# Optimization experiments

Measured on AMD Instinct MI355X. Metric: run time of the kernel, lower is better.

Reference implementation:

```python
import jax, jax.numpy as jnp
import numpy as np

N_HEADS = 16
HEAD = 64
HID = 1024
WIN = 256
LN_EPS = 1e-5


def _ln(x, g, b):
    m = jnp.mean(x, axis=-1, keepdims=True)
    v = jnp.mean((x - m) ** 2, axis=-1, keepdims=True)
    return (x - m) * jax.lax.rsqrt(v + LN_EPS) * g + b


def _window_shift(x):
    return jnp.concatenate([jnp.zeros_like(x[:, :WIN]), x[:, :-WIN]], axis=1)


def _additive_attn(x, vec, mask_add):
    B, S, _ = x.shape
    # per-head logits: (x * vec) summed within each head, scaled
    attn = (x * vec).reshape(B, S, N_HEADS, HEAD).sum(-1) / (HEAD ** 0.5)
    attn = jnp.exp(attn + mask_add)[..., None]          # [B,S,H,1]
    xh = x.reshape(B, S, N_HEADS, HEAD)
    s = jnp.cumsum(attn * xh, axis=1)
    s = s - _window_shift(s)                             # windowed cumsum of attn*x
    z = jnp.cumsum(attn, axis=1)
    z = z - _window_shift(z)                             # windowed cumsum of attn
    return (s / z).reshape(B, S, HID)


def setup_inputs():
    key = jax.random.key(0)
    ks = jax.random.split(key, 7)
    B, S = 4, 4096
    w = lambda k: (jax.random.normal(k, (HID, HID)) * 0.02).astype(jnp.float32)
    return {
        "hidden_states": jax.random.normal(ks[0], (B, S, HID), dtype=jnp.float32),
        "attention_mask": jnp.ones((B, S), dtype=jnp.float32),
        "Wq": w(ks[1]), "Wk": w(ks[2]), "Wv": w(ks[3]), "Wp": w(ks[4]),
        "query_attn": (jax.random.normal(ks[5], (HID,)) * 0.02).astype(jnp.float32),
        "key_attn": (jax.random.normal(ks[6], (HID,)) * 0.02).astype(jnp.float32),
        "ln1_g": jnp.ones((HID,), jnp.float32), "ln1_b": jnp.zeros((HID,), jnp.float32),
        "ln2_g": jnp.ones((HID,), jnp.float32), "ln2_b": jnp.zeros((HID,), jnp.float32),
    }


def reference(hidden_states, attention_mask, Wq, Wk, Wv, Wp, query_attn, key_attn,
              ln1_g, ln1_b, ln2_g, ln2_b):
    h = _ln(hidden_states, ln1_g, ln1_b)
    query = h @ Wq.T
    keys = h @ Wk.T
    values = h @ Wv.T
    mask_add = ((1.0 - attention_mask) * -10000.0)[:, :, None]  # [B,S,1]
    pooled_q = _additive_attn(query, query_attn, mask_add)
    pooled_q = pooled_q @ Wp.T                                  # (dropout is identity in eval)
    residual = h + pooled_q * keys
    mixed = _ln(residual, ln2_g, ln2_b)
    pooled_k = _additive_attn(mixed, key_attn, mask_add)
    return residual + pooled_k * values
```

## Files before the change

kernel.cpp:

```cpp
#include <hip/hip_runtime.h>
#include <hip/hip_bf16.h>

#define HID 1024
#define NH 16
#define HEAD 64
#define WIN 256
#define SEQ 4096
#define BATCH 4
#define NROWS (BATCH * SEQ)
#define LN_EPS 1e-5f

typedef unsigned short u16;
typedef __bf16 bf16x8 __attribute__((ext_vector_type(8)));
typedef float f32x4 __attribute__((ext_vector_type(4)));

static __device__ inline float bfu(u16 u) {
    union { unsigned int i; float f; } x;
    x.i = ((unsigned int)u) << 16;
    return x.f;
}

static __device__ inline u16 f2bf(float f) {
    union { float f; unsigned int i; } x;
    x.f = f;
    unsigned int lsb = (x.i >> 16) & 1u;
    x.i += 0x7fffu + lsb;
    return (u16)(x.i >> 16);
}

__global__ __launch_bounds__(256) void convert_weights(
    const float* __restrict__ wq, const float* __restrict__ wk,
    const float* __restrict__ wv, const float* __restrict__ wp,
    u16* __restrict__ o)
{
    int i = blockIdx.x * 256 + threadIdx.x;
    const int n = 1024 * 1024;
    if (i < n) {
        o[i]         = f2bf(wq[i]);
        o[n + i]     = f2bf(wk[i]);
        o[2 * n + i] = f2bf(wv[i]);
        o[3 * n + i] = f2bf(wp[i]);
    }
}

__global__ __launch_bounds__(256) void ln1_kernel(
    const float* __restrict__ x, const float* __restrict__ g,
    const float* __restrict__ b, u16* __restrict__ out)
{
    int row = blockIdx.x;
    int t = threadIdx.x;
    float4 v = ((const float4*)(x + (size_t)row * HID))[t];
    float s  = v.x + v.y + v.z + v.w;
    float ss = v.x * v.x + v.y * v.y + v.z * v.z + v.w * v.w;
    __shared__ float red[8];
    #pragma unroll
    for (int off = 32; off; off >>= 1) { s += __shfl_down(s, off); ss += __shfl_down(ss, off); }
    int wave = t >> 6, lane = t & 63;
    if (lane == 0) { red[wave] = s; red[4 + wave] = ss; }
    __syncthreads();
    float S  = red[0] + red[1] + red[2] + red[3];
    float SS = red[4] + red[5] + red[6] + red[7];
    float mean = S * (1.f / HID);
    float var  = SS * (1.f / HID) - mean * mean;
    float inv  = rsqrtf(var + LN_EPS);
    float4 gv = ((const float4*)g)[t];
    float4 bv = ((const float4*)b)[t];
    ushort4 o;
    o.x = f2bf((v.x - mean) * inv * gv.x + bv.x);
    o.y = f2bf((v.y - mean) * inv * gv.y + bv.y);
    o.z = f2bf((v.z - mean) * inv * gv.z + bv.z);
    o.w = f2bf((v.w - mean) * inv * gv.w + bv.w);
    ((ushort4*)(out + (size_t)row * HID))[t] = o;
}

#define GLDS(gp, lp) __builtin_amdgcn_global_load_lds( \
    (const __attribute__((address_space(1))) void*)(gp), \
    (__attribute__((address_space(3))) void*)(lp), 16, 0, 0)

#define PHASE(MH, KH, LOADB, STAGE_CODE, WAIT_CODE)                            \
  {                                                                            \
    if (LOADB) {                                                               \
      _Pragma("unroll") for (int n = 0; n < 4; ++n)                            \
        bF[n] = *(const bf16x8*)&rB[wc * 4096 +                                \
            (n * 16 + (lane & 15)) * 64 + ((c0 ^ ((KH) << 6)) >> 1)];          \
    }                                                                          \
    bf16x8 aF[4];                                                              \
    _Pragma("unroll") for (int i = 0; i < 4; ++i) {                            \
      const int mf = (MH) * 4 + i;                                             \
      aF[i] = *(const bf16x8*)&rA[(mf >> 1) * 4096 +                           \
          (wr * 32 + (mf & 1) * 16 + (lane & 15)) * 64 +                       \
          ((c0 ^ ((KH) << 6)) >> 1)];                                          \
    }                                                                          \
    STAGE_CODE                                                                 \
    WAIT_CODE                                                                  \
    __builtin_amdgcn_s_barrier();                                              \
    __builtin_amdgcn_sched_barrier(0);                                         \
    __builtin_amdgcn_s_setprio(1);                                             \
    _Pragma("unroll") for (int i = 0; i < 4; ++i)                              \
      _Pragma("unroll") for (int n = 0; n < 4; ++n)                            \
        acc[(MH) * 4 + i][n] = __builtin_amdgcn_mfma_f32_16x16x32_bf16(        \
            aF[i], bF[n], acc[(MH) * 4 + i][n], 0, 0, 0);                      \
    __builtin_amdgcn_s_setprio(0);                                             \
    __builtin_amdgcn_s_barrier();                                              \
    __builtin_amdgcn_sched_barrier(0);                                         \
  }

__global__ __launch_bounds__(512, 2) void gemm256(
    const u16* __restrict__ A, const u16* __restrict__ W,
    u16* __restrict__ C, int K, int ldc)
{
    __shared__ __align__(16) u16 sA[2][256 * 64];
    __shared__ __align__(16) u16 sB[2][256 * 64];

    const int tid = threadIdx.x;
    const int wgl = blockIdx.x >> 3;
    const int bm = (blockIdx.x & 7) * 8 + (wgl & 7);
    const int bn = wgl >> 3;

    const int wave = tid >> 6, lane = tid & 63;
    const int wr = wave >> 2, wc = wave & 3;

    const int rp = tid >> 3;
    const int colE = (((tid & 7) * 16) ^ ((rp & 7) << 4)) >> 1;
    const u16* gA = A + (size_t)(bm * 256 + (rp < 32 ? rp : rp + 96)) * K + colE;
    const u16* gB = W + (size_t)(bn * 256 + rp) * K + colE;

    const int c0 = ((lane >> 4) * 16) ^ ((lane & 7) << 4);

    f32x4 acc[8][4];
    #pragma unroll
    for (int m = 0; m < 8; ++m)
        #pragma unroll
        for (int n = 0; n < 4; ++n) {
            f32x4 z = {0.f, 0.f, 0.f, 0.f};
            acc[m][n] = z;
        }

    const int nk = K >> 6;

    #pragma unroll
    for (int w = 0; w < 4; ++w) GLDS(gB + (size_t)w * 64 * K, &sB[0][w * 4096 + tid * 8]);
    #pragma unroll
    for (int p = 0; p < 4; ++p) GLDS(gA + (size_t)p * 32 * K, &sA[0][p * 4096 + tid * 8]);
    asm volatile("s_waitcnt vmcnt(2)" ::: "memory");
    __builtin_amdgcn_s_barrier();
    __builtin_amdgcn_sched_barrier(0);

    for (int kt = 0; kt < nk; ++kt) {
        const int b = kt & 1;
        const u16* rA = sA[b];
        const u16* rB = sB[b];
        u16* dA = sA[b ^ 1];
        u16* dB = sB[b ^ 1];
        const bool pf = (kt + 1 < nk);
        const size_t ko = (size_t)(kt + 1) * 64;
        bf16x8 bF[4];

        PHASE(0, 0, true,
            { if (pf) { GLDS(gB + ko,                      &dB[0 * 4096 + tid * 8]);
                        GLDS(gB + (size_t)1 * 64 * K + ko, &dB[1 * 4096 + tid * 8]); } },
            { if (pf) asm volatile("s_waitcnt vmcnt(2)" ::: "memory");
              else    asm volatile("s_waitcnt vmcnt(0)" ::: "memory"); })
        PHASE(1, 0, false,
            { if (pf) { GLDS(gB + (size_t)2 * 64 * K + ko, &dB[2 * 4096 + tid * 8]);
                        GLDS(gB + (size_t)3 * 64 * K + ko, &dB[3 * 4096 + tid * 8]); } },
            { })
        PHASE(0, 1, true,
            { if (pf) { GLDS(gA + ko,                      &dA[0 * 4096 + tid * 8]);
                        GLDS(gA + (size_t)1 * 32 * K + ko, &dA[1 * 4096 + tid * 8]); } },
            { })
        PHASE(1, 1, false,
            { if (pf) { GLDS(gA + (size_t)2 * 32 * K + ko, &dA[2 * 4096 + tid * 8]);
                        GLDS(gA + (size_t)3 * 32 * K + ko, &dA[3 * 4096 + tid * 8]); } },
            { if (pf) asm volatile("s_waitcnt vmcnt(2)" ::: "memory"); })
    }

    #pragma unroll
    for (int mf = 0; mf < 8; ++mf) {
        int row0 = bm * 256 + wr * 128 + mf * 16 + ((lane >> 4) << 2);
        #pragma unroll
        for (int n = 0; n < 4; ++n) {
            int col = bn * 256 + wc * 64 + n * 16 + (lane & 15);
            #pragma unroll
            for (int r = 0; r < 4; ++r)
                C[(size_t)(row0 + r) * ldc + col] = f2bf(acc[mf][n][r]);
        }
    }
}

__global__ __launch_bounds__(256) void logits_kernel(
    const u16* __restrict__ x, int xstride,
    const float* __restrict__ vec, const float* __restrict__ mask,
    float* __restrict__ aw)
{
    int h = blockIdx.y, b = blockIdx.z;
    int s = blockIdx.x * 256 + threadIdx.x;
    __shared__ float vl[HEAD];
    if (threadIdx.x < HEAD) vl[threadIdx.x] = vec[h * HEAD + threadIdx.x];
    __syncthreads();
    const uint4* xr = (const uint4*)(x + ((size_t)(b * SEQ + s)) * xstride + h * HEAD);
    float dot = 0.f;
    #pragma unroll
    for (int i = 0; i < 8; ++i) {
        uint4 v = xr[i];
        const u16* p = (const u16*)&v;
        #pragma unroll
        for (int j = 0; j < 8; ++j) dot += bfu(p[j]) * vl[i * 8 + j];
    }
    float ma = (1.0f - mask[b * SEQ + s]) * -10000.0f;
    aw[((size_t)b * NH + h) * SEQ + s] = expf(dot * 0.125f + ma);
}

__global__ __launch_bounds__(256) void attn_win(
    const u16* __restrict__ x, int xstride,
    const float* __restrict__ aw_g,
    u16* __restrict__ out_bf,
    const u16* __restrict__ vsrc,
    float* __restrict__ outF,
    int fused)
{
    int c = blockIdx.x, h = blockIdx.y, b = blockIdx.z;
    __shared__ float awl[2][WIN];
    __shared__ float sts[2][4][HEAD];
    __shared__ float stz[2][4];

    int t = threadIdx.x, wave = t >> 6, lane = t & 63;
    bool havePrev = (c > 0);

    const float* awb = aw_g + ((size_t)b * NH + h) * SEQ;
    for (int i = t; i < 2 * WIN; i += 256) {
        int cc = i >> 8, j = i & (WIN - 1);
        float v = 0.f;
        if (cc == 1) v = awb[c * WIN + j];
        else if (havePrev) v = awb[(c - 1) * WIN + j];
        awl[cc][j] = v;
    }
    __syncthreads();

    const u16* xb = x + (size_t)b * SEQ * xstride + h * HEAD + lane;
    int jp0 = (havePrev ? (c - 1) : c) * WIN;
    int jc0 = c * WIN;
    int j0 = wave << 6;

    float s0 = 0.f, s1 = 0.f, z0 = 0.f, z1 = 0.f;
    #pragma unroll 8
    for (int jj = 0; jj < 64; ++jj) {
        int j = j0 + jj;
        float ap = awl[0][j], ac = awl[1][j];
        float xp = bfu(xb[(size_t)(jp0 + j) * xstride]);
        float xc = bfu(xb[(size_t)(jc0 + j) * xstride]);
        s0 += ap * xp; z0 += ap;
        s1 += ac * xc; z1 += ac;
    }
    sts[0][wave][lane] = s0;
    sts[1][wave][lane] = s1;
    if (lane == 0) { stz[0][wave] = z0; stz[1][wave] = z1; }
    __syncthreads();

    float cs0 = 0.f, cs1 = 0.f, cz0 = 0.f, cz1 = 0.f, tots = 0.f, totz = 0.f;
    #pragma unroll
    for (int w2 = 0; w2 < 4; ++w2) {
        float sp = sts[0][w2][lane], zp = stz[0][w2];
        tots += sp; totz += zp;
        if (w2 < wave) {
            cs0 += sp; cz0 += zp;
            cs1 += sts[1][w2][lane]; cz1 += stz[1][w2];
        }
    }

    float rp = cs0, rc = cs1, rzp = cz0, rzc = cz1;
    size_t obase = ((size_t)b * SEQ + c * WIN) * HID + h * HEAD + lane;
    size_t vbase = ((size_t)b * SEQ + c * WIN) * 3072 + 2048 + h * HEAD + lane;
    #pragma unroll 4
    for (int jj = 0; jj < 64; ++jj) {
        int j = j0 + jj;
        float ap = awl[0][j], ac = awl[1][j];
        float xp = bfu(xb[(size_t)(jp0 + j) * xstride]);
        float xc = bfu(xb[(size_t)(jc0 + j) * xstride]);
        rp += ap * xp; rzp += ap;
        rc += ac * xc; rzc += ac;
        float wv = (rc + tots - rp) / (rzc + totz - rzp);
        if (fused) {
            size_t oi = obase + (size_t)j * HID;
            outF[oi] = outF[oi] + wv * bfu(vsrc[vbase + (size_t)j * 3072]);
        } else {
            out_bf[obase + (size_t)j * HID] = f2bf(wv);
        }
    }
}

__global__ __launch_bounds__(256) void resid_ln2(
    const u16* h, const u16* __restrict__ qkv,
    const float* __restrict__ g, const float* __restrict__ b,
    const float* __restrict__ ka, const float* __restrict__ mask,
    float* __restrict__ residual, u16* mixed, float* __restrict__ aw2)
{
    int row = blockIdx.x;
    int t = threadIdx.x;
    ushort4 h4 = ((const ushort4*)(h + (size_t)row * HID))[t];
    ushort4 p4 = ((const ushort4*)(qkv + (size_t)row * 3072))[t];
    ushort4 k4 = ((const ushort4*)(qkv + (size_t)row * 3072 + 1024))[t];
    float r0 = bfu(h4.x) + bfu(p4.x) * bfu(k4.x);
    float r1 = bfu(h4.y) + bfu(p4.y) * bfu(k4.y);
    float r2 = bfu(h4.z) + bfu(p4.z) * bfu(k4.z);
    float r3 = bfu(h4.w) + bfu(p4.w) * bfu(k4.w);
    ((float4*)(residual + (size_t)row * HID))[t] = make_float4(r0, r1, r2, r3);

    float s  = r0 + r1 + r2 + r3;
    float ss = r0 * r0 + r1 * r1 + r2 * r2 + r3 * r3;
    __shared__ float red[8];
    #pragma unroll
    for (int off = 32; off; off >>= 1) { s += __shfl_down(s, off); ss += __shfl_down(ss, off); }
    int wave = t >> 6, lane = t & 63;
    if (lane == 0) { red[wave] = s; red[4 + wave] = ss; }
    __syncthreads();
    float S  = red[0] + red[1] + red[2] + red[3];
    float SS = red[4] + red[5] + red[6] + red[7];
    float mean = S * (1.f / HID);
    float var  = SS * (1.f / HID) - mean * mean;
    float inv  = rsqrtf(var + LN_EPS);
    float4 gv = ((const float4*)g)[t];
    float4 bv = ((const float4*)b)[t];
    float n0 = (r0 - mean) * inv * gv.x + bv.x;
    float n1 = (r1 - mean) * inv * gv.y + bv.y;
    float n2 = (r2 - mean) * inv * gv.z + bv.z;
    float n3 = (r3 - mean) * inv * gv.w + bv.w;
    ushort4 o;
    o.x = f2bf(n0); o.y = f2bf(n1); o.z = f2bf(n2); o.w = f2bf(n3);
    ((ushort4*)(mixed + (size_t)row * HID))[t] = o;

    float4 kv = ((const float4*)ka)[t];
    float partial = n0 * kv.x + n1 * kv.y + n2 * kv.z + n3 * kv.w;
    partial += __shfl_xor(partial, 1);
    partial += __shfl_xor(partial, 2);
    partial += __shfl_xor(partial, 4);
    partial += __shfl_xor(partial, 8);
    if ((t & 15) == 0) {
        int hh = t >> 4;
        int bb = row >> 12, sl = row & (SEQ - 1);
        float ma = (1.0f - mask[row]) * -10000.0f;
        aw2[((size_t)bb * NH + hh) * SEQ + sl] = expf(partial * 0.125f + ma);
    }
}

extern "C" void kernel_launch(void* const* d_in, const int* in_sizes, int n_in,
                              void* d_out, int out_size, void* d_ws, size_t ws_size,
                              hipStream_t stream)
{
    const float* hidden = (const float*)d_in[0];
    const float* mask   = (const float*)d_in[1];
    const float* Wq     = (const float*)d_in[2];
    const float* Wk     = (const float*)d_in[3];
    const float* Wv     = (const float*)d_in[4];
    const float* Wp     = (const float*)d_in[5];
    const float* qa     = (const float*)d_in[6];
    const float* ka     = (const float*)d_in[7];
    const float* g1     = (const float*)d_in[8];
    const float* b1     = (const float*)d_in[9];
    const float* g2     = (const float*)d_in[10];
    const float* b2     = (const float*)d_in[11];
    float* out = (float*)d_out;

    char* ws = (char*)d_ws;
    u16* wbf = (u16*)ws;       ws += (size_t)4 * 1024 * 1024 * 2;
    u16* hbf = (u16*)ws;       ws += (size_t)NROWS * HID * 2;
    u16* qkv = (u16*)ws;       ws += (size_t)NROWS * 3072 * 2;
    u16* pooled = (u16*)ws;    ws += (size_t)NROWS * HID * 2;
    float* aw1 = (float*)ws;   ws += (size_t)BATCH * NH * SEQ * 4;
    float* aw2 = (float*)ws;

    convert_weights<<<4096, 256, 0, stream>>>(Wq, Wk, Wv, Wp, wbf);
    ln1_kernel<<<NROWS, 256, 0, stream>>>(hidden, g1, b1, hbf);
    gemm256<<<768, 512, 0, stream>>>(hbf, wbf, qkv, HID, 3072);
    logits_kernel<<<dim3(SEQ / 256, NH, BATCH), 256, 0, stream>>>(qkv, 3072, qa, mask, aw1);
    attn_win<<<dim3(SEQ / WIN, NH, BATCH), 256, 0, stream>>>(qkv, 3072, aw1, pooled,
                                                             (const u16*)nullptr, (float*)nullptr, 0);
    gemm256<<<256, 512, 0, stream>>>(pooled, wbf + (size_t)3 * 1024 * 1024, qkv, HID, 3072);
    resid_ln2<<<NROWS, 256, 0, stream>>>(hbf, qkv, g2, b2, ka, mask, out, hbf, aw2);
    attn_win<<<dim3(SEQ / WIN, NH, BATCH), 256, 0, stream>>>(hbf, HID, aw2, pooled,
                                                             qkv, out, 1);
}
```

Before: 329.3 us.

## Fuse LN1 with weight conversion, persistent GEMM, two-head attention, bf16 residual

Merges the weight conversion into the LN1 launch. The QKV GEMM becomes persistent: 256 blocks loop over 768 tiles and prefetch the next tile's first K-slice while writing the current tile's output. The windowed attention kernel now handles two heads per 512-thread block with packed 2-element loads and stores. The residual is stored as bf16 into the free Q slot of qkv instead of a float32 write to the output. The final kernel then writes out in a single pass with no float read-modify-write. The goals are fewer launches, less tail imbalance and less memory traffic. The cost is bf16 rounding of the residual, which adds precision loss to the final output.

```diff
diff --git a/kernel.cpp b/kernel.cpp
--- a/kernel.cpp
+++ b/kernel.cpp
@@ -28,31 +28,28 @@
     return (u16)(x.i >> 16);
 }
 
-__global__ __launch_bounds__(256) void convert_weights(
+__global__ __launch_bounds__(256) void ln1_conv(
+    const float* __restrict__ x, const float* __restrict__ g,
+    const float* __restrict__ b, u16* __restrict__ out,
     const float* __restrict__ wq, const float* __restrict__ wk,
     const float* __restrict__ wv, const float* __restrict__ wp,
-    u16* __restrict__ o)
-{
-    int i = blockIdx.x * 256 + threadIdx.x;
-    const int n = 1024 * 1024;
-    if (i < n) {
-        o[i]         = f2bf(wq[i]);
-        o[n + i]     = f2bf(wk[i]);
-        o[2 * n + i] = f2bf(wv[i]);
-        o[3 * n + i] = f2bf(wp[i]);
-    }
-}
-
-__global__ __launch_bounds__(256) void ln1_kernel(
-    const float* __restrict__ x, const float* __restrict__ g,
-    const float* __restrict__ b, u16* __restrict__ out)
-{
+    u16* __restrict__ wo)
+{
+    __shared__ float red[8];
+    int t = threadIdx.x;
+    if (blockIdx.x >= NROWS) {
+        int i = (blockIdx.x - NROWS) * 256 + t;
+        const int n = 1024 * 1024;
+        wo[i]         = f2bf(wq[i]);
+        wo[n + i]     = f2bf(wk[i]);
+        wo[2 * n + i] = f2bf(wv[i]);
+        wo[3 * n + i] = f2bf(wp[i]);
+        return;
+    }
     int row = blockIdx.x;
-    int t = threadIdx.x;
     float4 v = ((const float4*)(x + (size_t)row * HID))[t];
     float s  = v.x + v.y + v.z + v.w;
     float ss = v.x * v.x + v.y * v.y + v.z * v.z + v.w * v.w;
-    __shared__ float red[8];
     #pragma unroll
     for (int off = 32; off; off >>= 1) { s += __shfl_down(s, off); ss += __shfl_down(ss, off); }
     int wave = t >> 6, lane = t & 63;
@@ -107,84 +104,101 @@
 
 __global__ __launch_bounds__(512, 2) void gemm256(
     const u16* __restrict__ A, const u16* __restrict__ W,
-    u16* __restrict__ C, int K, int ldc)
+    u16* __restrict__ C, int K, int ldc, int ntiles)
 {
     __shared__ __align__(16) u16 sA[2][256 * 64];
     __shared__ __align__(16) u16 sB[2][256 * 64];
 
     const int tid = threadIdx.x;
-    const int wgl = blockIdx.x >> 3;
-    const int bm = (blockIdx.x & 7) * 8 + (wgl & 7);
-    const int bn = wgl >> 3;
-
     const int wave = tid >> 6, lane = tid & 63;
     const int wr = wave >> 2, wc = wave & 3;
 
     const int rp = tid >> 3;
+    const int rowA = (rp < 32 ? rp : rp + 96);
     const int colE = (((tid & 7) * 16) ^ ((rp & 7) << 4)) >> 1;
-    const u16* gA = A + (size_t)(bm * 256 + (rp < 32 ? rp : rp + 96)) * K + colE;
+    const int c0 = ((lane >> 4) * 16) ^ ((lane & 7) << 4);
+
+    const int nk = K >> 6;
+
+    int a = blockIdx.x;
+    int wgl = a >> 3;
+    int bm = (a & 7) * 8 + (wgl & 7);
+    int bn = wgl >> 3;
+    const u16* gA = A + (size_t)(bm * 256 + rowA) * K + colE;
     const u16* gB = W + (size_t)(bn * 256 + rp) * K + colE;
-
-    const int c0 = ((lane >> 4) * 16) ^ ((lane & 7) << 4);
-
-    f32x4 acc[8][4];
-    #pragma unroll
-    for (int m = 0; m < 8; ++m)
+    #pragma unroll
+    for (int w = 0; w < 4; ++w) GLDS(gB + (size_t)w * 64 * K, &sB[0][w * 4096 + tid * 8]);
+    #pragma unroll
+    for (int p = 0; p < 4; ++p) GLDS(gA + (size_t)p * 32 * K, &sA[0][p * 4096 + tid * 8]);
+
+    while (true) {
+        asm volatile("s_waitcnt vmcnt(2)" ::: "memory");
+        __builtin_amdgcn_s_barrier();
+        __builtin_amdgcn_sched_barrier(0);
+
+        f32x4 acc[8][4];
         #pragma unroll
-        for (int n = 0; n < 4; ++n) {
-            f32x4 z = {0.f, 0.f, 0.f, 0.f};
-            acc[m][n] = z;
+        for (int m = 0; m < 8; ++m)
+            #pragma unroll
+            for (int n = 0; n < 4; ++n) {
+                f32x4 z = {0.f, 0.f, 0.f, 0.f};
+                acc[m][n] = z;
+            }
+
+        for (int kt = 0; kt < nk; ++kt) {
+            const int b = kt & 1;
+            const u16* rA = sA[b];
+            const u16* rB = sB[b];
+            u16* dA = sA[b ^ 1];
+            u16* dB = sB[b ^ 1];
+            const bool pf = (kt + 1 < nk);
+            const size_t ko = (size_t)(kt + 1) * 64;
+            bf16x8 bF[4];
+
+            PHASE(0, 0, true,
+                { if (pf) { GLDS(gB + ko,                      &dB[0 * 4096 + tid * 8]);
+                            GLDS(gB + (size_t)1 * 64 * K + ko, &dB[1 * 4096 + tid * 8]); } },
+                { if (pf) asm volatile("s_waitcnt vmcnt(2)" ::: "memory");
+                  else    asm volatile("s_waitcnt vmcnt(0)" ::: "memory"); })
+            PHASE(1, 0, false,
+                { if (pf) { GLDS(gB + (size_t)2 * 64 * K + ko, &dB[2 * 4096 + tid * 8]);
+                            GLDS(gB + (size_t)3 * 64 * K + ko, &dB[3 * 4096 + tid * 8]); } },
+                { })
+            PHASE(0, 1, true,
+                { if (pf) { GLDS(gA + ko,                      &dA[0 * 4096 + tid * 8]);
+                            GLDS(gA + (size_t)1 * 32 * K + ko, &dA[1 * 4096 + tid * 8]); } },
+                { })
+            PHASE(1, 1, false,
+                { if (pf) { GLDS(gA + (size_t)2 * 32 * K + ko, &dA[2 * 4096 + tid * 8]);
+                            GLDS(gA + (size_t)3 * 32 * K + ko, &dA[3 * 4096 + tid * 8]); } },
+                { if (pf) asm volatile("s_waitcnt vmcnt(2)" ::: "memory"); })
         }
 
-    const int nk = K >> 6;
-
-    #pragma unroll
-    for (int w = 0; w < 4; ++w) GLDS(gB + (size_t)w * 64 * K, &sB[0][w * 4096 + tid * 8]);
-    #pragma unroll
-    for (int p = 0; p < 4; ++p) GLDS(gA + (size_t)p * 32 * K, &sA[0][p * 4096 + tid * 8]);
-    asm volatile("s_waitcnt vmcnt(2)" ::: "memory");
-    __builtin_amdgcn_s_barrier();
-    __builtin_amdgcn_sched_barrier(0);
-
-    for (int kt = 0; kt < nk; ++kt) {
-        const int b = kt & 1;
-        const u16* rA = sA[b];
-        const u16* rB = sB[b];
-        u16* dA = sA[b ^ 1];
-        u16* dB = sB[b ^ 1];
-        const bool pf = (kt + 1 < nk);
-        const size_t ko = (size_t)(kt + 1) * 64;
-        bf16x8 bF[4];
-
-        PHASE(0, 0, true,
-            { if (pf) { GLDS(gB + ko,                      &dB[0 * 4096 + tid * 8]);
-                        GLDS(gB + (size_t)1 * 64 * K + ko, &dB[1 * 4096 + tid * 8]); } },
-            { if (pf) asm volatile("s_waitcnt vmcnt(2)" ::: "memory");
-              else    asm volatile("s_waitcnt vmcnt(0)" ::: "memory"); })
-        PHASE(1, 0, false,
-            { if (pf) { GLDS(gB + (size_t)2 * 64 * K + ko, &dB[2 * 4096 + tid * 8]);
-                        GLDS(gB + (size_t)3 * 64 * K + ko, &dB[3 * 4096 + tid * 8]); } },
-            { })
-        PHASE(0, 1, true,
-            { if (pf) { GLDS(gA + ko,                      &dA[0 * 4096 + tid * 8]);
-                        GLDS(gA + (size_t)1 * 32 * K + ko, &dA[1 * 4096 + tid * 8]); } },
-            { })
-        PHASE(1, 1, false,
-            { if (pf) { GLDS(gA + (size_t)2 * 32 * K + ko, &dA[2 * 4096 + tid * 8]);
-                        GLDS(gA + (size_t)3 * 32 * K + ko, &dA[3 * 4096 + tid * 8]); } },
-            { if (pf) asm volatile("s_waitcnt vmcnt(2)" ::: "memory"); })
-    }
-
-    #pragma unroll
-    for (int mf = 0; mf < 8; ++mf) {
-        int row0 = bm * 256 + wr * 128 + mf * 16 + ((lane >> 4) << 2);
+        const int bmC = bm, bnC = bn;
+        a += gridDim.x;
+        const bool more = (a < ntiles);
+        if (more) {
+            wgl = a >> 3; bm = (a & 7) * 8 + (wgl & 7); bn = wgl >> 3;
+            gA = A + (size_t)(bm * 256 + rowA) * K + colE;
+            gB = W + (size_t)(bn * 256 + rp) * K + colE;
+            #pragma unroll
+            for (int w = 0; w < 4; ++w) GLDS(gB + (size_t)w * 64 * K, &sB[0][w * 4096 + tid * 8]);
+            #pragma unroll
+            for (int p = 0; p < 4; ++p) GLDS(gA + (size_t)p * 32 * K, &sA[0][p * 4096 + tid * 8]);
+        }
+
         #pragma unroll
-        for (int n = 0; n < 4; ++n) {
-            int col = bn * 256 + wc * 64 + n * 16 + (lane & 15);
+        for (int mf = 0; mf < 8; ++mf) {
+            int row0 = bmC * 256 + wr * 128 + mf * 16 + ((lane >> 4) << 2);
             #pragma unroll
-            for (int r = 0; r < 4; ++r)
-                C[(size_t)(row0 + r) * ldc + col] = f2bf(acc[mf][n][r]);
+            for (int n = 0; n < 4; ++n) {
+                int col = bnC * 256 + wc * 64 + n * 16 + (lane & 15);
+                #pragma unroll
+                for (int r = 0; r < 4; ++r)
+                    C[(size_t)(row0 + r) * ldc + col] = f2bf(acc[mf][n][r]);
+            }
         }
+        if (!more) break;
     }
 }
 
@@ -211,89 +225,101 @@
     aw[((size_t)b * NH + h) * SEQ + s] = expf(dot * 0.125f + ma);
 }
 
-__global__ __launch_bounds__(256) void attn_win(
+__global__ __launch_bounds__(512) void attn_win2(
     const u16* __restrict__ x, int xstride,
     const float* __restrict__ aw_g,
     u16* __restrict__ out_bf,
-    const u16* __restrict__ vsrc,
+    const u16* __restrict__ resv,
     float* __restrict__ outF,
     int fused)
 {
-    int c = blockIdx.x, h = blockIdx.y, b = blockIdx.z;
-    __shared__ float awl[2][WIN];
-    __shared__ float sts[2][4][HEAD];
-    __shared__ float stz[2][4];
+    int c = blockIdx.x, h2 = blockIdx.y, b = blockIdx.z;
+    __shared__ float awl[2][2][WIN];
+    __shared__ float2 sts[2][8][64];
+    __shared__ float stz[2][8][2];
 
     int t = threadIdx.x, wave = t >> 6, lane = t & 63;
+    int hh = lane >> 5;
+    int coff = hh * 64 + (lane & 31) * 2;
     bool havePrev = (c > 0);
 
-    const float* awb = aw_g + ((size_t)b * NH + h) * SEQ;
-    for (int i = t; i < 2 * WIN; i += 256) {
-        int cc = i >> 8, j = i & (WIN - 1);
+    const float* aw0 = aw_g + ((size_t)b * NH + h2 * 2) * SEQ;
+    for (int i = t; i < 1024; i += 512) {
+        int hd = i >> 9, cc = (i >> 8) & 1, j = i & 255;
         float v = 0.f;
-        if (cc == 1) v = awb[c * WIN + j];
-        else if (havePrev) v = awb[(c - 1) * WIN + j];
-        awl[cc][j] = v;
+        if (cc == 1) v = aw0[hd * SEQ + c * WIN + j];
+        else if (havePrev) v = aw0[hd * SEQ + (c - 1) * WIN + j];
+        awl[hd][cc][j] = v;
     }
     __syncthreads();
 
-    const u16* xb = x + (size_t)b * SEQ * xstride + h * HEAD + lane;
-    int jp0 = (havePrev ? (c - 1) : c) * WIN;
+    const u16* xb = x + (size_t)b * SEQ * xstride + h2 * 128 + coff;
+    int jp0 = (havePrev ? c - 1 : c) * WIN;
     int jc0 = c * WIN;
-    int j0 = wave << 6;
-
-    float s0 = 0.f, s1 = 0.f, z0 = 0.f, z1 = 0.f;
+    int j0 = wave * 32;
+
+    float s0a = 0, s0b = 0, s1a = 0, s1b = 0, z0 = 0, z1 = 0;
     #pragma unroll 8
-    for (int jj = 0; jj < 64; ++jj) {
+    for (int jj = 0; jj < 32; ++jj) {
         int j = j0 + jj;
-        float ap = awl[0][j], ac = awl[1][j];
-        float xp = bfu(xb[(size_t)(jp0 + j) * xstride]);
-        float xc = bfu(xb[(size_t)(jc0 + j) * xstride]);
-        s0 += ap * xp; z0 += ap;
-        s1 += ac * xc; z1 += ac;
-    }
-    sts[0][wave][lane] = s0;
-    sts[1][wave][lane] = s1;
-    if (lane == 0) { stz[0][wave] = z0; stz[1][wave] = z1; }
+        float ap = awl[hh][0][j], ac = awl[hh][1][j];
+        unsigned up = *(const unsigned*)(xb + (size_t)(jp0 + j) * xstride);
+        unsigned uc = *(const unsigned*)(xb + (size_t)(jc0 + j) * xstride);
+        s0a += ap * bfu(up & 0xffff); s0b += ap * bfu(up >> 16); z0 += ap;
+        s1a += ac * bfu(uc & 0xffff); s1b += ac * bfu(uc >> 16); z1 += ac;
+    }
+    sts[0][wave][lane] = make_float2(s0a, s0b);
+    sts[1][wave][lane] = make_float2(s1a, s1b);
+    if ((lane & 31) == 0) { stz[0][wave][hh] = z0; stz[1][wave][hh] = z1; }
     __syncthreads();
 
-    float cs0 = 0.f, cs1 = 0.f, cz0 = 0.f, cz1 = 0.f, tots = 0.f, totz = 0.f;
-    #pragma unroll
-    for (int w2 = 0; w2 < 4; ++w2) {
-        float sp = sts[0][w2][lane], zp = stz[0][w2];
-        tots += sp; totz += zp;
+    float cs0a = 0, cs0b = 0, cs1a = 0, cs1b = 0, cz0 = 0, cz1 = 0;
+    float totsa = 0, totsb = 0, totz = 0;
+    #pragma unroll
+    for (int w2 = 0; w2 < 8; ++w2) {
+        float2 sp = sts[0][w2][lane];
+        float zp = stz[0][w2][hh];
+        totsa += sp.x; totsb += sp.y; totz += zp;
         if (w2 < wave) {
-            cs0 += sp; cz0 += zp;
-            cs1 += sts[1][w2][lane]; cz1 += stz[1][w2];
+            cs0a += sp.x; cs0b += sp.y; cz0 += zp;
+            float2 sc = sts[1][w2][lane];
+            cs1a += sc.x; cs1b += sc.y; cz1 += stz[1][w2][hh];
         }
     }
 
-    float rp = cs0, rc = cs1, rzp = cz0, rzc = cz1;
-    size_t obase = ((size_t)b * SEQ + c * WIN) * HID + h * HEAD + lane;
-    size_t vbase = ((size_t)b * SEQ + c * WIN) * 3072 + 2048 + h * HEAD + lane;
+    float rpa = cs0a, rpb = cs0b, rca = cs1a, rcb = cs1b, rzp = cz0, rzc = cz1;
+    size_t rowbase = (size_t)b * SEQ + jc0;
     #pragma unroll 4
-    for (int jj = 0; jj < 64; ++jj) {
+    for (int jj = 0; jj < 32; ++jj) {
         int j = j0 + jj;
-        float ap = awl[0][j], ac = awl[1][j];
-        float xp = bfu(xb[(size_t)(jp0 + j) * xstride]);
-        float xc = bfu(xb[(size_t)(jc0 + j) * xstride]);
-        rp += ap * xp; rzp += ap;
-        rc += ac * xc; rzc += ac;
-        float wv = (rc + tots - rp) / (rzc + totz - rzp);
+        float ap = awl[hh][0][j], ac = awl[hh][1][j];
+        unsigned up = *(const unsigned*)(xb + (size_t)(jp0 + j) * xstride);
+        unsigned uc = *(const unsigned*)(xb + (size_t)(jc0 + j) * xstride);
+        rpa += ap * bfu(up & 0xffff); rpb += ap * bfu(up >> 16); rzp += ap;
+        rca += ac * bfu(uc & 0xffff); rcb += ac * bfu(uc >> 16); rzc += ac;
+        float inv = 1.f / (rzc + totz - rzp);
+        float wva = (rca + totsa - rpa) * inv;
+        float wvb = (rcb + totsb - rpb) * inv;
         if (fused) {
-            size_t oi = obase + (size_t)j * HID;
-            outF[oi] = outF[oi] + wv * bfu(vsrc[vbase + (size_t)j * 3072]);
+            size_t roff = (rowbase + j) * 3072 + h2 * 128 + coff;
+            unsigned rr = *(const unsigned*)(resv + roff);
+            unsigned vv = *(const unsigned*)(resv + roff + 2048);
+            float2 o;
+            o.x = bfu(rr & 0xffff) + wva * bfu(vv & 0xffff);
+            o.y = bfu(rr >> 16)    + wvb * bfu(vv >> 16);
+            *(float2*)(outF + (rowbase + j) * HID + h2 * 128 + coff) = o;
         } else {
-            out_bf[obase + (size_t)j * HID] = f2bf(wv);
+            unsigned pk = (unsigned)f2bf(wva) | ((unsigned)f2bf(wvb) << 16);
+            *(unsigned*)(out_bf + (rowbase + j) * HID + h2 * 128 + coff) = pk;
         }
     }
 }
 
 __global__ __launch_bounds__(256) void resid_ln2(
-    const u16* h, const u16* __restrict__ qkv,
+    const u16* h, u16* qkv,
     const float* __restrict__ g, const float* __restrict__ b,
     const float* __restrict__ ka, const float* __restrict__ mask,
-    float* __restrict__ residual, u16* mixed, float* __restrict__ aw2)
+    u16* mixed, float* __restrict__ aw2)
 {
     int row = blockIdx.x;
     int t = threadIdx.x;
@@ -304,7 +330,9 @@
     float r1 = bfu(h4.y) + bfu(p4.y) * bfu(k4.y);
     float r2 = bfu(h4.z) + bfu(p4.z) * bfu(k4.z);
     float r3 = bfu(h4.w) + bfu(p4.w) * bfu(k4.w);
-    ((float4*)(residual + (size_t)row * HID))[t] = make_float4(r0, r1, r2, r3);
+    ushort4 rb;
+    rb.x = f2bf(r0); rb.y = f2bf(r1); rb.z = f2bf(r2); rb.w = f2bf(r3);
+    ((ushort4*)(qkv + (size_t)row * 3072))[t] = rb;
 
     float s  = r0 + r1 + r2 + r3;
     float ss = r0 * r0 + r1 * r1 + r2 * r2 + r3 * r3;
@@ -369,14 +397,13 @@
     float* aw1 = (float*)ws;   ws += (size_t)BATCH * NH * SEQ * 4;
     float* aw2 = (float*)ws;
 
-    convert_weights<<<4096, 256, 0, stream>>>(Wq, Wk, Wv, Wp, wbf);
-    ln1_kernel<<<NROWS, 256, 0, stream>>>(hidden, g1, b1, hbf);
-    gemm256<<<768, 512, 0, stream>>>(hbf, wbf, qkv, HID, 3072);
+    ln1_conv<<<NROWS + 4096, 256, 0, stream>>>(hidden, g1, b1, hbf, Wq, Wk, Wv, Wp, wbf);
+    gemm256<<<256, 512, 0, stream>>>(hbf, wbf, qkv, HID, 3072, 768);
     logits_kernel<<<dim3(SEQ / 256, NH, BATCH), 256, 0, stream>>>(qkv, 3072, qa, mask, aw1);
-    attn_win<<<dim3(SEQ / WIN, NH, BATCH), 256, 0, stream>>>(qkv, 3072, aw1, pooled,
-                                                             (const u16*)nullptr, (float*)nullptr, 0);
-    gemm256<<<256, 512, 0, stream>>>(pooled, wbf + (size_t)3 * 1024 * 1024, qkv, HID, 3072);
-    resid_ln2<<<NROWS, 256, 0, stream>>>(hbf, qkv, g2, b2, ka, mask, out, hbf, aw2);
-    attn_win<<<dim3(SEQ / WIN, NH, BATCH), 256, 0, stream>>>(hbf, HID, aw2, pooled,
-                                                             qkv, out, 1);
-}
+    attn_win2<<<dim3(SEQ / WIN, NH / 2, BATCH), 512, 0, stream>>>(
+        qkv, 3072, aw1, pooled, (const u16*)nullptr, (float*)nullptr, 0);
+    gemm256<<<256, 512, 0, stream>>>(pooled, wbf + (size_t)3 * 1024 * 1024, qkv, HID, 3072, 256);
+    resid_ln2<<<NROWS, 256, 0, stream>>>(hbf, qkv, g2, b2, ka, mask, hbf, aw2);
+    attn_win2<<<dim3(SEQ / WIN, NH / 2, BATCH), 512, 0, stream>>>(
+        hbf, HID, aw2, (u16*)nullptr, qkv, out, 1);
+}
```

New measurement: 274.7 us. -16.6%, faster.
